# Kernel tuning notes

Hardware: AMD Instinct MI355X
Metric: run time of the kernel (lower is better)

## Reference

```python
import jax, jax.numpy as jnp
import numpy as np

WP = 1.0     # warp_penalty
TEMP = 0.01  # soft-min temperature
BIG = 1e7    # finite stand-in for +inf (exp(-BIG/TEMP) == 0 exactly in fp32)


def setup_inputs() -> dict:
    key = jax.random.key(0)
    k1, k2, k3, k4 = jax.random.split(key, 4)
    B, T1, T2, C = 8, 256, 1024, 128
    fea_a = jax.random.normal(k1, (B, T1, C), jnp.float32)
    fea_b = jax.random.normal(k2, (B, T2, C), jnp.float32)
    len_a = jax.random.randint(k3, (B,), T1 // 2, T1 + 1)
    len_b = jax.random.randint(k4, (B,), T2 // 2, T2 + 1)
    return {"fea_a": fea_a, "len_a": len_a, "fea_b": fea_b, "len_b": len_b}


def _softmin(v, temp):
    # v: [3, B, T1]; stable -temp*log(sum(exp(-v/temp)))
    m = jnp.min(v, axis=0)
    return m - temp * jnp.log(jnp.sum(jnp.exp(-(v - m) / temp), axis=0))


def _soft_dtw(fea_a, fea_b, len_a, len_b, wp=WP, temp=TEMP):
    B, T1, C = fea_a.shape
    T2 = fea_b.shape[1]
    # L1 cost: [B, T2, T1]  (rows index fea_b, cols index fea_a, as in torch code)
    cost = jnp.mean(jnp.abs(fea_a[:, None, :, :] - fea_b[:, :, None, :]), axis=-1)
    # skewed cost: skew[b, d, j] = cost[b, clip(d-j, 0, T2-1), j]
    D = T1 + T2 - 1
    d = jnp.arange(D)[:, None]
    j = jnp.arange(T1)[None, :]
    idx = jnp.clip(d - j, 0, T2 - 1)           # [D, T1]
    skew = cost[:, idx, j]                      # [B, D, T1]
    skew = jnp.swapaxes(skew, 0, 1)             # [D, B, T1] for scan

    pc0 = jnp.full((B, T1 + 1), BIG, jnp.float32)       # path_cost (diag d-1)
    pcp0 = pc0.at[:, 0].set(0.0)                         # path_cost_prev (diag d-2)

    def step(carry, crow):
        pc, pcp = carry
        dirs = jnp.stack([pcp[:, :-1], pc[:, 1:] + wp, pc[:, :-1] + wp], axis=0)
        new = crow + _softmin(dirs, temp)                # [B, T1]
        new = jnp.concatenate([jnp.full((B, 1), BIG, new.dtype), new], axis=1)
        return (new, pc), new

    _, ys = jax.lax.scan(step, (pc0, pcp0), skew)        # ys: [D, B, T1+1]
    # per-sample answer: diagonal len_a+len_b-2, entry len_a
    di = len_a + len_b - 2
    loss_i = ys[di, jnp.arange(B), len_a]
    return jnp.sum(loss_i)  # reduction='mean' over a length-1 accumulator == sum


def reference(fea_a, len_a, fea_b, len_b):
    return _soft_dtw(fea_a, fea_b, len_a, len_b)
```

## Files before the change

### kernel.cpp

```cpp
#include <hip/hip_runtime.h>
#include <hip/hip_bf16.h>
#include <hip/hip_fp16.h>
#include <cstddef>
#include <cstdint>

#define BIGV 10000000.0f
#define WPV  1.0f

#define BATCH 8
#define T1N 256
#define T2N 1024
#define CN 128
#define DN 1279

#define FLAG_MAGIC 0x600D0000

typedef __attribute__((ext_vector_type(2))) _Float16 half2v;

__global__ __launch_bounds__(256) void cost_kernel(const float* __restrict__ A,
                                                   const float* __restrict__ Bf,
                                                   const int* __restrict__ lenA,
                                                   const int* __restrict__ lenB,
                                                   float* __restrict__ sk) {
    __shared__ char As[64 * 256];
    __shared__ char Bs[127 * 256];

    const int b  = blockIdx.z;
    const int d0 = blockIdx.y * 64;
    const int j0 = blockIdx.x * 64;
    const int tid = threadIdx.x;

    const int dEnd = lenA[b] + lenB[b] - 2;
    if (d0 > dEnd) return;

    const float* Ab = A  + (size_t)b * T1N * CN;
    const float* Bb = Bf + (size_t)b * T2N * CN;

    const int tj = tid & 15;
    const int td = tid >> 4;
    const int brow0 = td - tj + 63;
    const int rbase = d0 - j0 - 63;

#define SWB(row, g) (((row) << 8) + ((((g) + (row)) & 15) << 4))

    #pragma unroll
    for (int i = 0; i < 8; ++i) {
        int idx = tid + i * 256;
        int row = idx >> 5;
        int q   = idx & 31;
        float4 f = *(const float4*)(Ab + (size_t)(j0 + row) * CN + (q << 2));
        half2v h0 = { (_Float16)f.x, (_Float16)f.y };
        half2v h1 = { (_Float16)f.z, (_Float16)f.w };
        char* dst = As + SWB(row, q >> 1) + ((q & 1) << 3);
        ((uint32_t*)dst)[0] = __builtin_bit_cast(uint32_t, h0);
        ((uint32_t*)dst)[1] = __builtin_bit_cast(uint32_t, h1);
    }
    #pragma unroll
    for (int i = 0; i < 16; ++i) {
        int idx = tid + i * 256;
        if (idx < 4064) {
            int row = idx >> 5;
            int q   = idx & 31;
            int gr = rbase + row;
            gr = gr < 0 ? 0 : (gr > T2N - 1 ? T2N - 1 : gr);
            float4 f = *(const float4*)(Bb + (size_t)gr * CN + (q << 2));
            half2v h0 = { (_Float16)f.x, (_Float16)f.y };
            half2v h1 = { (_Float16)f.z, (_Float16)f.w };
            char* dst = Bs + SWB(row, q >> 1) + ((q & 1) << 3);
            ((uint32_t*)dst)[0] = __builtin_bit_cast(uint32_t, h0);
            ((uint32_t*)dst)[1] = __builtin_bit_cast(uint32_t, h1);
        }
    }
    __syncthreads();

    float acc[4][4];
    #pragma unroll
    for (int i = 0; i < 4; ++i)
        #pragma unroll
        for (int j = 0; j < 4; ++j) acc[i][j] = 0.0f;

    const half2v one2 = { (_Float16)1.0f, (_Float16)1.0f };

    for (int g = 0; g < 16; ++g) {
        uint4 a4[4], bv[7];
        #pragma unroll
        for (int ji = 0; ji < 4; ++ji) {
            int row = tj + 16 * ji;
            a4[ji] = *(const uint4*)(As + SWB(row, g));
        }
        #pragma unroll
        for (int m = 0; m < 7; ++m) {
            int row = brow0 + 16 * (m - 3);
            bv[m] = *(const uint4*)(Bs + SWB(row, g));
        }
        #pragma unroll
        for (int dk = 0; dk < 4; ++dk) {
            #pragma unroll
            for (int ji = 0; ji < 4; ++ji) {
                uint4 au = a4[ji];
                uint4 bu = bv[dk - ji + 3];
                float a = acc[dk][ji];
                #pragma unroll
                for (int w = 0; w < 4; ++w) {
                    uint32_t ua = (&au.x)[w];
                    uint32_t ub = (&bu.x)[w];
                    half2v d2 = __builtin_bit_cast(half2v, ua)
                              - __builtin_bit_cast(half2v, ub);
                    uint32_t du = __builtin_bit_cast(uint32_t, d2) & 0x7FFF7FFFu;
#if __has_builtin(__builtin_amdgcn_fdot2)
                    a = __builtin_amdgcn_fdot2(__builtin_bit_cast(half2v, du),
                                               one2, a, false);
#else
                    half2v ad = __builtin_bit_cast(half2v, du);
                    a += (float)ad.x + (float)ad.y;
#endif
                }
                acc[dk][ji] = a;
            }
        }
    }
#undef SWB

    #pragma unroll
    for (int dk = 0; dk < 4; ++dk) {
        int d = d0 + td + 16 * dk;
        if (d < DN) {
            size_t rowoff = ((size_t)b * DN + d) * T1N;
            #pragma unroll
            for (int ji = 0; ji < 4; ++ji) {
                int j = j0 + tj + 16 * ji;
                sk[rowoff + j] = acc[dk][ji] * (1.0f / 128.0f);
            }
        }
    }
}

__device__ __forceinline__ float min3f(float a, float b, float c) {
    float d;
    asm("v_min3_f32 %0, %1, %2, %3" : "=v"(d) : "v"(a), "v"(b), "v"(c));
    return d;
}

__global__ __launch_bounds__(64, 1) void dp_lds_kernel(const float* __restrict__ sk,
                                                       const int* __restrict__ lenA,
                                                       const int* __restrict__ lenB,
                                                       float* __restrict__ partials,
                                                       int* __restrict__ flags,
                                                       float* __restrict__ out) {
    __shared__ char ring[3 * 16384];

    const int b = blockIdx.x;
    const int L = threadIdx.x;

    const int la = __builtin_amdgcn_readfirstlane(lenA[b]);
    const int lb = __builtin_amdgcn_readfirstlane(lenB[b]);
    const int dEnd = la + lb - 2;
    const int kLast = dEnd >> 4;

    const float* skb = sk + (size_t)b * DN * T1N + (L << 2);

    char* s0 = ring;
    char* s1 = ring + 16384;
    char* s2 = ring + 32768;

    float x0 = BIGV, x1 = BIGV, x2 = BIGV, x3 = BIGV;
    float y0 = BIGV, y1 = BIGV, y2 = BIGV, y3 = BIGV;
    float pp = (L == 0) ? 0.0f : BIGV;

#define SHFL_UP1(SRC)                                                       \
    __int_as_float(__builtin_amdgcn_update_dpp(                             \
        __float_as_int(BIGV), __float_as_int(SRC),                          \
        0x138 , 0xF, 0xF, false))

#define WAITV(N) do {                                                       \
        asm volatile("s_waitcnt vmcnt(" #N ")" ::: "memory");               \
        __builtin_amdgcn_sched_barrier(0);                                  \
    } while (0)

#define WAITL0 do {                                                         \
        asm volatile("s_waitcnt lgkmcnt(0)" ::: "memory");                  \
        __builtin_amdgcn_sched_barrier(0);                                  \
    } while (0)

#define ISSUE(KB, SL) do {                                                  \
        _Pragma("unroll")                                                   \
        for (int r_ = 0; r_ < 16; ++r_) {                                   \
            int row_ = ((KB) << 4) + r_;                                    \
            row_ = row_ > DN - 1 ? DN - 1 : row_;                           \
            __builtin_amdgcn_global_load_lds(                               \
                (const __attribute__((address_space(1))) void*)(skb + (size_t)row_ * T1N), \
                (__attribute__((address_space(3))) void*)((SL) + (r_ << 10)), \
                16, 0, 0);                                                  \
        }                                                                   \
    } while (0)

#define READ16(SL)                                                          \
        float4 cc0  = *(const float4*)((SL) +  0 * 1024 + (L << 4));        \
        float4 cc1  = *(const float4*)((SL) +  1 * 1024 + (L << 4));        \
        float4 cc2  = *(const float4*)((SL) +  2 * 1024 + (L << 4));        \
        float4 cc3  = *(const float4*)((SL) +  3 * 1024 + (L << 4));        \
        float4 cc4  = *(const float4*)((SL) +  4 * 1024 + (L << 4));        \
        float4 cc5  = *(const float4*)((SL) +  5 * 1024 + (L << 4));        \
        float4 cc6  = *(const float4*)((SL) +  6 * 1024 + (L << 4));        \
        float4 cc7  = *(const float4*)((SL) +  7 * 1024 + (L << 4));        \
        float4 cc8  = *(const float4*)((SL) +  8 * 1024 + (L << 4));        \
        float4 cc9  = *(const float4*)((SL) +  9 * 1024 + (L << 4));        \
        float4 cc10 = *(const float4*)((SL) + 10 * 1024 + (L << 4));        \
        float4 cc11 = *(const float4*)((SL) + 11 * 1024 + (L << 4));        \
        float4 cc12 = *(const float4*)((SL) + 12 * 1024 + (L << 4));        \
        float4 cc13 = *(const float4*)((SL) + 13 * 1024 + (L << 4));        \
        float4 cc14 = *(const float4*)((SL) + 14 * 1024 + (L << 4));        \
        float4 cc15 = *(const float4*)((SL) + 15 * 1024 + (L << 4));

#define DPP_STEP(C4, P, Q) do {                                             \
        float4 c_ = (C4);                                                   \
        float p1_ = SHFL_UP1(P##3);                                         \
        float w0_ = P##0 + WPV, w1_ = P##1 + WPV;                           \
        float w2_ = P##2 + WPV, w3_ = P##3 + WPV;                           \
        float wp_ = p1_ + WPV;                                              \
        float t0_ = c_.x + min3f(pp, w0_, wp_);                             \
        float t1_ = c_.y + min3f(Q##0, w1_, w0_);                           \
        float t2_ = c_.z + min3f(Q##1, w2_, w1_);                           \
        float t3_ = c_.w + min3f(Q##2, w3_, w2_);                           \
        pp = p1_;                                                           \
        Q##0 = t0_; Q##1 = t1_; Q##2 = t2_; Q##3 = t3_;                     \
    } while (0)

#define COMPUTE16 do {                                                      \
        DPP_STEP(cc0,  x, y); DPP_STEP(cc1,  y, x);                         \
        DPP_STEP(cc2,  x, y); DPP_STEP(cc3,  y, x);                         \
        DPP_STEP(cc4,  x, y); DPP_STEP(cc5,  y, x);                         \
        DPP_STEP(cc6,  x, y); DPP_STEP(cc7,  y, x);                         \
        DPP_STEP(cc8,  x, y); DPP_STEP(cc9,  y, x);                         \
        DPP_STEP(cc10, x, y); DPP_STEP(cc11, y, x);                         \
        DPP_STEP(cc12, x, y); DPP_STEP(cc13, y, x);                         \
        DPP_STEP(cc14, x, y); DPP_STEP(cc15, y, x);                         \
    } while (0)

#define GSTEP(C4, PN, QN, R) do { if ((R) <= rem) DPP_STEP(C4, PN, QN); } while (0)
#define GUARD16 do {                                                        \
        GSTEP(cc0,  x, y, 0);  GSTEP(cc1,  y, x, 1);                        \
        GSTEP(cc2,  x, y, 2);  GSTEP(cc3,  y, x, 3);                        \
        GSTEP(cc4,  x, y, 4);  GSTEP(cc5,  y, x, 5);                        \
        GSTEP(cc6,  x, y, 6);  GSTEP(cc7,  y, x, 7);                        \
        GSTEP(cc8,  x, y, 8);  GSTEP(cc9,  y, x, 9);                        \
        GSTEP(cc10, x, y, 10); GSTEP(cc11, y, x, 11);                       \
        GSTEP(cc12, x, y, 12); GSTEP(cc13, y, x, 13);                       \
        GSTEP(cc14, x, y, 14); GSTEP(cc15, y, x, 15);                       \
    } while (0)

    ISSUE(0, s0);
    ISSUE(1, s1);
    ISSUE(2, s2);

    int k = 0;
    for (; k + 2 < kLast; ++k) {
        WAITV(32);
        READ16(s0);
        WAITL0;
        ISSUE(k + 3, s0);
        COMPUTE16;
        { char* t_ = s0; s0 = s1; s1 = s2; s2 = t_; }
    }

    {
        WAITV(32);
        READ16(s0);
        WAITL0;
        COMPUTE16;
        { char* t_ = s0; s0 = s1; s1 = s2; s2 = t_; }
    }
    {
        WAITV(16);
        READ16(s0);
        WAITL0;
        COMPUTE16;
        { char* t_ = s0; s0 = s1; s1 = s2; s2 = t_; }
    }
    const int rem = dEnd & 15;
    {
        WAITV(0);
        READ16(s0);
        GUARD16;
    }

    float f0, f1, f2, f3;
    if ((rem & 1) == 0) { f0 = y0; f1 = y1; f2 = y2; f3 = y3; }
    else                { f0 = x0; f1 = x1; f2 = x2; f3 = x3; }

    const int tcap = la - 1;
    if (L == (tcap >> 2)) {
        const int kk = tcap & 3;
        float r = f0;
        if (kk == 1) r = f1;
        else if (kk == 2) r = f2;
        else if (kk == 3) r = f3;
        partials[b] = r;
        __threadfence();
        __hip_atomic_store(&flags[b], FLAG_MAGIC + b,
                           __ATOMIC_RELEASE, __HIP_MEMORY_SCOPE_AGENT);
    }

    if (b == 0 && L == 0) {
        float s = 0.0f;
        for (int i = 0; i < BATCH; ++i) {
            while (__hip_atomic_load(&flags[i], __ATOMIC_ACQUIRE,
                                     __HIP_MEMORY_SCOPE_AGENT) != FLAG_MAGIC + i)
                __builtin_amdgcn_s_sleep(2);
            s += __hip_atomic_load(&partials[i], __ATOMIC_RELAXED,
                                   __HIP_MEMORY_SCOPE_AGENT);
        }
        out[0] = s;
    }
#undef GUARD16
#undef GSTEP
#undef COMPUTE16
#undef DPP_STEP
#undef READ16
#undef ISSUE
#undef WAITL0
#undef WAITV
#undef SHFL_UP1
}

extern "C" void kernel_launch(void* const* d_in, const int* in_sizes, int n_in,
                              void* d_out, int out_size, void* d_ws, size_t ws_size,
                              hipStream_t stream) {
    const float* feaA = (const float*)d_in[0];
    const int*   lenA = (const int*)d_in[1];
    const float* feaB = (const float*)d_in[2];
    const int*   lenB = (const int*)d_in[3];

    float* sk       = (float*)d_ws;
    float* partials = (float*)((char*)d_ws + (size_t)BATCH * DN * T1N * sizeof(float));
    int*   flags    = (int*)(partials + BATCH);

    cost_kernel<<<dim3(T1N / 64, (DN + 63) / 64, BATCH), 256, 0, stream>>>(feaA, feaB, lenA, lenB, sk);
    dp_lds_kernel<<<BATCH, 64, 0, stream>>>(sk, lenA, lenB, partials, flags, (float*)d_out);
}
```

Baseline: 143.0 us.

## Process anti-diagonals in pairs to shorten DP dependency chain

Rewrites the wavefront DP step to advance two anti-diagonals at once, computing the second diagonal's candidate terms from precomputed cost-plus-min sums of the first. Both cross-lane DPP shifts for the previous diagonals are issued up front, so the serial latency per diagonal is reduced. A peeled first block and a scalar-step tail handle alignment and the remainder. This adds more instructions per pair and more bookkeeping for the parity of the final result.

```diff
diff --git a/kernel.cpp b/kernel.cpp
--- a/kernel.cpp
+++ b/kernel.cpp
@@ -141,12 +141,12 @@
     return d;
 }
 
-__global__ __launch_bounds__(64, 1) void dp_lds_kernel(const float* __restrict__ sk,
-                                                       const int* __restrict__ lenA,
-                                                       const int* __restrict__ lenB,
-                                                       float* __restrict__ partials,
-                                                       int* __restrict__ flags,
-                                                       float* __restrict__ out) {
+__global__ __launch_bounds__(64, 1) void dp_ldspair_kernel(const float* __restrict__ sk,
+                                                           const int* __restrict__ lenA,
+                                                           const int* __restrict__ lenB,
+                                                           float* __restrict__ partials,
+                                                           int* __restrict__ flags,
+                                                           float* __restrict__ out) {
     __shared__ char ring[3 * 16384];
 
     const int b = blockIdx.x;
@@ -163,8 +163,8 @@
     char* s1 = ring + 16384;
     char* s2 = ring + 32768;
 
-    float x0 = BIGV, x1 = BIGV, x2 = BIGV, x3 = BIGV;
-    float y0 = BIGV, y1 = BIGV, y2 = BIGV, y3 = BIGV;
+    float p1_0 = BIGV, p1_1 = BIGV, p1_2 = BIGV, p1_3 = BIGV;
+    float p2_0 = BIGV, p2_1 = BIGV, p2_2 = BIGV, p2_3 = BIGV;
     float pp = (L == 0) ? 0.0f : BIGV;
 
 #define SHFL_UP1(SRC)                                                       \
@@ -212,89 +212,120 @@
         float4 cc14 = *(const float4*)((SL) + 14 * 1024 + (L << 4));        \
         float4 cc15 = *(const float4*)((SL) + 15 * 1024 + (L << 4));
 
-#define DPP_STEP(C4, P, Q) do {                                             \
+#define SSTEP(C4) do {                                                      \
         float4 c_ = (C4);                                                   \
-        float p1_ = SHFL_UP1(P##3);                                         \
-        float w0_ = P##0 + WPV, w1_ = P##1 + WPV;                           \
-        float w2_ = P##2 + WPV, w3_ = P##3 + WPV;                           \
-        float wp_ = p1_ + WPV;                                              \
-        float t0_ = c_.x + min3f(pp, w0_, wp_);                             \
-        float t1_ = c_.y + min3f(Q##0, w1_, w0_);                           \
-        float t2_ = c_.z + min3f(Q##1, w2_, w1_);                           \
-        float t3_ = c_.w + min3f(Q##2, w3_, w2_);                           \
-        pp = p1_;                                                           \
-        Q##0 = t0_; Q##1 = t1_; Q##2 = t2_; Q##3 = t3_;                     \
-    } while (0)
-
-#define COMPUTE16 do {                                                      \
-        DPP_STEP(cc0,  x, y); DPP_STEP(cc1,  y, x);                         \
-        DPP_STEP(cc2,  x, y); DPP_STEP(cc3,  y, x);                         \
-        DPP_STEP(cc4,  x, y); DPP_STEP(cc5,  y, x);                         \
-        DPP_STEP(cc6,  x, y); DPP_STEP(cc7,  y, x);                         \
-        DPP_STEP(cc8,  x, y); DPP_STEP(cc9,  y, x);                         \
-        DPP_STEP(cc10, x, y); DPP_STEP(cc11, y, x);                         \
-        DPP_STEP(cc12, x, y); DPP_STEP(cc13, y, x);                         \
-        DPP_STEP(cc14, x, y); DPP_STEP(cc15, y, x);                         \
-    } while (0)
-
-#define GSTEP(C4, PN, QN, R) do { if ((R) <= rem) DPP_STEP(C4, PN, QN); } while (0)
-#define GUARD16 do {                                                        \
-        GSTEP(cc0,  x, y, 0);  GSTEP(cc1,  y, x, 1);                        \
-        GSTEP(cc2,  x, y, 2);  GSTEP(cc3,  y, x, 3);                        \
-        GSTEP(cc4,  x, y, 4);  GSTEP(cc5,  y, x, 5);                        \
-        GSTEP(cc6,  x, y, 6);  GSTEP(cc7,  y, x, 7);                        \
-        GSTEP(cc8,  x, y, 8);  GSTEP(cc9,  y, x, 9);                        \
-        GSTEP(cc10, x, y, 10); GSTEP(cc11, y, x, 11);                       \
-        GSTEP(cc12, x, y, 12); GSTEP(cc13, y, x, 13);                       \
-        GSTEP(cc14, x, y, 14); GSTEP(cc15, y, x, 15);                       \
-    } while (0)
+        float pone_ = SHFL_UP1(p1_3);                                       \
+        float w0_ = p1_0 + WPV, w1_ = p1_1 + WPV;                           \
+        float w2_ = p1_2 + WPV, w3_ = p1_3 + WPV;                           \
+        float wp_ = pone_ + WPV;                                            \
+        float n0_ = c_.x + min3f(pp, w0_, wp_);                             \
+        float n1_ = c_.y + min3f(p2_0, w1_, w0_);                           \
+        float n2_ = c_.z + min3f(p2_1, w2_, w1_);                           \
+        float n3_ = c_.w + min3f(p2_2, w3_, w2_);                           \
+        pp = pone_;                                                         \
+        p2_0 = p1_0; p2_1 = p1_1; p2_2 = p1_2; p2_3 = p1_3;                 \
+        p1_0 = n0_;  p1_1 = n1_;  p1_2 = n2_;  p1_3 = n3_;                  \
+    } while (0)
+
+#define PAIR(CA, CB) do {                                                   \
+        float s1_ = SHFL_UP1(p1_3);                                         \
+        float t1_ = SHFL_UP1(p2_3);                                         \
+        float w0_ = p1_0 + WPV, w1_ = p1_1 + WPV;                           \
+        float w2_ = p1_2 + WPV, w3_ = p1_3 + WPV;                           \
+        float ws_ = s1_ + WPV;                                              \
+        float q0_ = min3f(t1_,  w0_, ws_);                                  \
+        float q1_ = min3f(p2_0, w1_, w0_);                                  \
+        float q2_ = min3f(p2_1, w2_, w1_);                                  \
+        float q3_ = min3f(p2_2, w3_, w2_);                                  \
+        float4 ca_ = (CA), cb_ = (CB);                                      \
+        float g0_ = ca_.x + WPV, g1_ = ca_.y + WPV;                         \
+        float g2_ = ca_.z + WPV, g3_ = ca_.w + WPV;                         \
+        float m20_ = g0_ + q0_, m21_ = g1_ + q1_;                           \
+        float m22_ = g2_ + q2_, m23_ = g3_ + q3_;                           \
+        float u_ = SHFL_UP1(m23_);                                          \
+        float h0_ = min3f(s1_,  m20_, u_);                                  \
+        float h1_ = min3f(p1_0, m21_, m20_);                                \
+        float h2_ = min3f(p1_1, m22_, m21_);                                \
+        float h3_ = min3f(p1_2, m23_, m22_);                                \
+        p2_0 = ca_.x + q0_; p2_1 = ca_.y + q1_;                             \
+        p2_2 = ca_.z + q2_; p2_3 = ca_.w + q3_;                             \
+        p1_0 = cb_.x + h0_; p1_1 = cb_.y + h1_;                             \
+        p1_2 = cb_.z + h2_; p1_3 = cb_.w + h3_;                             \
+    } while (0)
+
+#define PAIR8 do {                                                          \
+        PAIR(cc0,  cc1);  PAIR(cc2,  cc3);                                  \
+        PAIR(cc4,  cc5);  PAIR(cc6,  cc7);                                  \
+        PAIR(cc8,  cc9);  PAIR(cc10, cc11);                                 \
+        PAIR(cc12, cc13); PAIR(cc14, cc15);                                 \
+    } while (0)
+
+#define GS(C4, R) do { if ((R) <= rem) SSTEP(C4); } while (0)
+#define TAIL do {                                                           \
+        pp = SHFL_UP1(p2_3);       \
+        GS(cc0, 0);   GS(cc1, 1);   GS(cc2, 2);   GS(cc3, 3);               \
+        GS(cc4, 4);   GS(cc5, 5);   GS(cc6, 6);   GS(cc7, 7);               \
+        GS(cc8, 8);   GS(cc9, 9);   GS(cc10, 10); GS(cc11, 11);             \
+        GS(cc12, 12); GS(cc13, 13); GS(cc14, 14); GS(cc15, 15);             \
+    } while (0)
+
+#define ROT { char* t_ = s0; s0 = s1; s1 = s2; s2 = t_; }
 
     ISSUE(0, s0);
     ISSUE(1, s1);
     ISSUE(2, s2);
 
-    int k = 0;
+    {
+        WAITV(32);
+        READ16(s0);
+        WAITL0;
+        ISSUE(3, s0);
+        SSTEP(cc0); SSTEP(cc1);
+        PAIR(cc2,  cc3);  PAIR(cc4,  cc5);
+        PAIR(cc6,  cc7);  PAIR(cc8,  cc9);
+        PAIR(cc10, cc11); PAIR(cc12, cc13);
+        PAIR(cc14, cc15);
+        ROT;
+    }
+
+    int k = 1;
     for (; k + 2 < kLast; ++k) {
         WAITV(32);
         READ16(s0);
         WAITL0;
         ISSUE(k + 3, s0);
-        COMPUTE16;
-        { char* t_ = s0; s0 = s1; s1 = s2; s2 = t_; }
+        PAIR8;
+        ROT;
     }
 
     {
         WAITV(32);
         READ16(s0);
         WAITL0;
-        COMPUTE16;
-        { char* t_ = s0; s0 = s1; s1 = s2; s2 = t_; }
+        PAIR8;
+        ROT;
     }
     {
         WAITV(16);
         READ16(s0);
         WAITL0;
-        COMPUTE16;
-        { char* t_ = s0; s0 = s1; s1 = s2; s2 = t_; }
+        PAIR8;
+        ROT;
     }
     const int rem = dEnd & 15;
     {
         WAITV(0);
         READ16(s0);
-        GUARD16;
-    }
-
-    float f0, f1, f2, f3;
-    if ((rem & 1) == 0) { f0 = y0; f1 = y1; f2 = y2; f3 = y3; }
-    else                { f0 = x0; f1 = x1; f2 = x2; f3 = x3; }
+        TAIL;
+    }
 
     const int tcap = la - 1;
     if (L == (tcap >> 2)) {
         const int kk = tcap & 3;
-        float r = f0;
-        if (kk == 1) r = f1;
-        else if (kk == 2) r = f2;
-        else if (kk == 3) r = f3;
+        float r = p1_0;
+        if (kk == 1) r = p1_1;
+        else if (kk == 2) r = p1_2;
+        else if (kk == 3) r = p1_3;
         partials[b] = r;
         __threadfence();
         __hip_atomic_store(&flags[b], FLAG_MAGIC + b,
@@ -312,10 +343,12 @@
         }
         out[0] = s;
     }
-#undef GUARD16
-#undef GSTEP
-#undef COMPUTE16
-#undef DPP_STEP
+#undef ROT
+#undef TAIL
+#undef GS
+#undef PAIR8
+#undef PAIR
+#undef SSTEP
 #undef READ16
 #undef ISSUE
 #undef WAITL0
@@ -336,5 +369,5 @@
     int*   flags    = (int*)(partials + BATCH);
 
     cost_kernel<<<dim3(T1N / 64, (DN + 63) / 64, BATCH), 256, 0, stream>>>(feaA, feaB, lenA, lenB, sk);
-    dp_lds_kernel<<<BATCH, 64, 0, stream>>>(sk, lenA, lenB, partials, flags, (float*)d_out);
+    dp_ldspair_kernel<<<BATCH, 64, 0, stream>>>(sk, lenA, lenB, partials, flags, (float*)d_out);
 }
```

Result: slower. 148.5 us (+3.9%).
